# Optimization experiments

Measured on AMD Instinct MI355X. Metric: run time of the kernel, lower is better.

## Reference

```python
import jax, jax.numpy as jnp
import numpy as np

B, CIN, COUT, WID, M1, M2, H, W = 8, 3, 3, 16, 8, 8, 256, 256


def _fftfreq(n, d):
    # torch.fft.fftfreq(n, d); d may be a traced scalar
    k = np.concatenate([np.arange(0, (n - 1) // 2 + 1), np.arange(-(n // 2), 0)]).astype(np.float32)
    return jnp.asarray(k) / (n * d)


def _cplx(ri):
    return jax.lax.complex(ri[..., 0], ri[..., 1])


def _inorm(v, eps=1e-5):
    # InstanceNorm2d, affine=False: normalize over spatial dims per (b, c)
    mu = jnp.mean(v, axis=(-2, -1), keepdims=True)
    var = jnp.var(v, axis=(-2, -1), keepdims=True)
    return (v - mu) * jax.lax.rsqrt(var + eps)


def setup_inputs() -> dict:
    key = jax.random.key(0)
    ks = jax.random.split(key, 13)
    scale = 1.0 / (WID * WID)
    u = lambda k, s: scale * (0.5 + 0.5 * jax.random.uniform(k, s, jnp.float32))
    return {
        "x": jax.random.normal(ks[0], (B, CIN, H, W), jnp.float32),
        "fc0_w": jax.random.normal(ks[1], (CIN + 2, WID), jnp.float32) * 0.1,
        "fc0_b": jax.random.normal(ks[2], (WID,), jnp.float32) * 0.01,
        "pole1_ri": u(ks[3], (WID, WID, M1, 2)),
        "pole2_ri": u(ks[4], (WID, WID, M2, 2)),
        "residue_ri": u(ks[5], (WID, WID, M1, M2, 2)),
        "w0_w": jax.random.normal(ks[6], (WID, WID), jnp.float32) * 0.1,
        "w0_b": jax.random.normal(ks[7], (WID,), jnp.float32) * 0.01,
        "fc1_w": jax.random.normal(ks[8], (WID, 128), jnp.float32) * 0.1,
        "fc1_b": jax.random.normal(ks[9], (128,), jnp.float32) * 0.01,
        "fc2_w": jax.random.normal(ks[10], (128, COUT), jnp.float32) * 0.1,
        "fc2_b": jax.random.normal(ks[11], (COUT,), jnp.float32) * 0.01,
        "tx": jnp.linspace(0.0, 1.0, W, dtype=jnp.float32).reshape(1, W),
        "ty": jnp.linspace(0.0, 1.0, H, dtype=jnp.float32).reshape(1, H),
    }


def _pr2d(v, p1, p2, res, tx, ty):
    # v: [b, i, h, w] real; p1:[i,k,m1], p2:[i,k,m2], res:[i,k,m1,m2] complex
    b, i, h, w = v.shape
    dty = ty[0, 1] - ty[0, 0]
    dtx = tx[0, 1] - tx[0, 0]
    alpha = jnp.fft.fft2(v)  # [b,i,h,w] complex64
    lam1 = (2j * jnp.pi) * _fftfreq(h, dty)  # [h]
    lam2 = (2j * jnp.pi) * _fftfreq(w, dtx)  # [w]
    A1 = 1.0 / (lam1[None, None, None, :] - p1[..., None])  # [i,k,p,h]
    A2 = 1.0 / (lam2[None, None, None, :] - p2[..., None])  # [i,k,q,w]
    # output_residue1[b,k,o,x] = sum_{i,p,q} alpha[b,i,o,x] res[i,k,p,q] A1[i,k,p,o] A2[i,k,q,x]
    T = jnp.einsum('ikpq,ikpo->ikqo', res, A1)
    G = jnp.einsum('ikqo,ikqx->ikox', T, A2)        # [i,k,h,w] pole-residue transfer kernel
    out1 = jnp.einsum('biox,ikox->bkox', alpha, G)
    x1 = jnp.fft.ifft2(out1).real
    # output_residue2[b,k,p,q] = sum_{i,o,x} alpha[b,i,o,x] res[i,k,p,q] A1[i,k,p,o] A2[i,k,q,x]
    S = jnp.einsum('biox,ikqx->bikoq', alpha, A2)
    Mt = jnp.einsum('bikoq,ikpo->bikpq', S, A1)
    out2 = jnp.einsum('bikpq,ikpq->bkpq', Mt, res)  # [b,k,m1,m2]
    # transient part: x2[n,i,z,x] = sum_{b,p,q} out2[n,b,p,q] exp(p1[b,i,p] ty[z]) exp(p2[b,i,q] tx[x])
    tyc = ty.reshape(-1).astype(p1.dtype)
    txc = tx.reshape(-1).astype(p2.dtype)
    E1 = jnp.exp(p1[..., None] * tyc)  # [i,k,p,h]
    E2 = jnp.exp(p2[..., None] * txc)  # [i,k,q,w]
    U = jnp.einsum('nbpq,bipz->nbiqz', out2, E1)
    x2 = jnp.einsum('nbiqz,biqx->nizx', U, E2).real / (w * h)
    return x1 + x2


def reference(x, fc0_w, fc0_b, pole1_ri, pole2_ri, residue_ri, w0_w, w0_b,
              fc1_w, fc1_b, fc2_w, fc2_b, tx, ty):
    b, c, h, w = x.shape
    v = jnp.transpose(x, (0, 2, 3, 1))  # [b,h,w,c]
    gx = jnp.broadcast_to(jnp.linspace(0.0, 1.0, h, dtype=x.dtype)[None, :, None, None], (b, h, w, 1))
    gy = jnp.broadcast_to(jnp.linspace(0.0, 1.0, w, dtype=x.dtype)[None, None, :, None], (b, h, w, 1))
    v = jnp.concatenate([v, gx, gy], axis=-1)
    v = v @ fc0_w + fc0_b                 # [b,h,w,width]
    v = jnp.transpose(v, (0, 3, 1, 2))    # [b,width,h,w]
    p1, p2, res = _cplx(pole1_ri), _cplx(pole2_ri), _cplx(residue_ri)
    x1 = _inorm(_pr2d(_inorm(v), p1, p2, res, tx, ty))
    x2 = jnp.einsum('bihw,oi->bohw', v, w0_w) + w0_b[None, :, None, None]  # 1x1 conv
    u = x1 + x2
    u = jnp.transpose(u, (0, 2, 3, 1))
    u = jnp.sin(u @ fc1_w + fc1_b)
    u = u @ fc2_w + fc2_b
    return jnp.transpose(u, (0, 3, 1, 2))
```

## Files before the change

### kernel.cpp

```cpp
#include <hip/hip_runtime.h>
#include <cstddef>

#define NPIX 65536
#define PI_F 3.14159265358979323846f

__device__ __forceinline__ void cacc(float2& acc, float2 a, float2 b) {
  acc.x = fmaf(a.x, b.x, fmaf(-a.y, b.y, acc.x));
  acc.y = fmaf(a.x, b.y, fmaf(a.y, b.x, acc.y));
}
__device__ __forceinline__ float2 cmulf(float2 a, float2 b) {
  return make_float2(a.x*b.x - a.y*b.y, a.x*b.y + a.y*b.x);
}
__device__ __forceinline__ float2 add2(float2 a, float2 b) { return make_float2(a.x+b.x, a.y+b.y); }
__device__ __forceinline__ float2 sub2(float2 a, float2 b) { return make_float2(a.x-b.x, a.y-b.y); }
__device__ __forceinline__ float2 shflc(float2 v, int mask) {
  return make_float2(__shfl_xor(v.x, mask), __shfl_xor(v.y, mask));
}
__device__ __forceinline__ void make_tw(float sgn, int l, float2* tw) {
  const float c = sgn * (2.0f*PI_F/256.0f);
  int idxs[8] = { l, 64+l, 2*l, (l&31)<<2, (l&15)<<3, (l&7)<<4, (l&3)<<5, (l&1)<<6 };
  #pragma unroll
  for (int r = 0; r < 8; ++r) { float sn, cs; __sincosf(c*idxs[r], &sn, &cs); tw[r] = make_float2(cs, sn); }
}
__device__ __forceinline__ void fwd_stage(float2& vv, int lane, int H, float2 tws, bool unit) {
  float2 p = shflc(vv, H);
  bool up = (lane & H) != 0;
  float2 lo = add2(vv, p);
  float2 df = sub2(p, vv);
  float2 hi = unit ? df : cmulf(df, tws);
  vv = up ? hi : lo;
}
__device__ __forceinline__ void inv_stage(float2& vv, int lane, int H, float2 tws, bool unit) {
  float2 p = shflc(vv, H);
  bool up = (lane & H) != 0;
  float2 bv = up ? vv : p;
  float2 av = up ? p : vv;
  float2 t = unit ? bv : cmulf(bv, tws);
  vv = up ? sub2(av, t) : add2(av, t);
}
__device__ __forceinline__ void ifft256_reg(float2& v0, float2& v1, float2& v2,
    float2& v3, int lane, const float2* tw) {
  inv_stage(v0, lane, 1, tw[0], true ); inv_stage(v1, lane, 1, tw[0], true );
  inv_stage(v2, lane, 1, tw[0], true ); inv_stage(v3, lane, 1, tw[0], true );
  inv_stage(v0, lane, 2, tw[7], false); inv_stage(v1, lane, 2, tw[7], false);
  inv_stage(v2, lane, 2, tw[7], false); inv_stage(v3, lane, 2, tw[7], false);
  inv_stage(v0, lane, 4, tw[6], false); inv_stage(v1, lane, 4, tw[6], false);
  inv_stage(v2, lane, 4, tw[6], false); inv_stage(v3, lane, 4, tw[6], false);
  inv_stage(v0, lane, 8, tw[5], false); inv_stage(v1, lane, 8, tw[5], false);
  inv_stage(v2, lane, 8, tw[5], false); inv_stage(v3, lane, 8, tw[5], false);
  inv_stage(v0, lane, 16, tw[4], false); inv_stage(v1, lane, 16, tw[4], false);
  inv_stage(v2, lane, 16, tw[4], false); inv_stage(v3, lane, 16, tw[4], false);
  inv_stage(v0, lane, 32, tw[3], false); inv_stage(v1, lane, 32, tw[3], false);
  inv_stage(v2, lane, 32, tw[3], false); inv_stage(v3, lane, 32, tw[3], false);
  { float2 t01 = cmulf(v1, tw[2]); float2 n0 = add2(v0, t01), n1 = sub2(v0, t01);
    float2 t23 = cmulf(v3, tw[2]); float2 n2 = add2(v2, t23), n3 = sub2(v2, t23);
    v0 = n0; v1 = n1; v2 = n2; v3 = n3; }
  { float2 t02 = cmulf(v2, tw[0]); float2 n0 = add2(v0, t02), n2 = sub2(v0, t02);
    float2 t13 = cmulf(v3, tw[1]); float2 n1 = add2(v1, t13), n3 = sub2(v1, t13);
    v0 = n0; v2 = n2; v1 = n1; v3 = n3; }
}

__global__ __launch_bounds__(256) void k_setup(const float2* __restrict__ p1,
    const float2* __restrict__ p2, const float* __restrict__ txv,
    const float* __restrict__ tyv, float2* __restrict__ A1,
    float2* __restrict__ A2T, float2* __restrict__ A2L,
    float2* __restrict__ E1, float2* __restrict__ E2) {
  int gid = blockIdx.x*256 + threadIdx.x;
  int o = gid & 255, p = (gid>>8)&7, k = (gid>>11)&15, i = gid>>15;
  float ko = (o < 128) ? (float)o : (float)(o - 256);
  float dty = tyv[1] - tyv[0];
  float dtx = txv[1] - txv[0];
  const float TWO_PI = 6.283185307179586f;
  {
    float lam = TWO_PI * ko / (256.0f * dty);
    float2 pv = p1[(i*16+k)*8 + p];
    float xr = -pv.x, yi = lam - pv.y;
    float D = xr*xr + yi*yi;
    A1[((size_t)((i*16+k)*8 + p))*256 + o] = make_float2(xr/D, -yi/D);
    float tv = tyv[o];
    float m = expf(pv.x*tv);
    E1[((size_t)((i*16+k)*8 + p))*256 + o] = make_float2(m*cosf(pv.y*tv), m*sinf(pv.y*tv));
  }
  {
    int fo = __brev((unsigned)o) >> 24;
    float ko2 = (fo < 128) ? (float)fo : (float)(fo - 256);
    float lam = TWO_PI * ko2 / (256.0f * dtx);
    float2 pv = p2[(i*16+k)*8 + p];
    float xr = -pv.x, yi = lam - pv.y;
    float D = xr*xr + yi*yi;
    float2 val = make_float2(xr/D, -yi/D);
    A2T[((size_t)i*256 + o)*128 + k*8 + p] = val;
    A2L[((size_t)((i*16+k)*8 + p))*256 + o] = val;
    float tv = txv[o];
    float m = expf(pv.x*tv);
    E2[((size_t)((i*16+k)*8 + p))*256 + o] = make_float2(m*cosf(pv.y*tv), m*sinf(pv.y*tv));
  }
}

__global__ __launch_bounds__(256) void k_T(const float2* __restrict__ res,
    const float2* __restrict__ A1, float2* __restrict__ Tt) {
  int ik = blockIdx.x, tid = threadIdx.x;
  __shared__ float2 rbuf[64];
  __shared__ float2 a1[8][256];
  if (tid < 64) rbuf[tid] = res[(size_t)ik*64 + tid];
  for (int e = 0; e < 8; ++e) {
    int lin = tid + 256*e;
    int p = lin >> 8, o = lin & 255;
    a1[p][o] = A1[((size_t)ik*8 + p)*256 + o];
  }
  __syncthreads();
  int o = tid;
  #pragma unroll
  for (int q = 0; q < 8; ++q) {
    float2 acc = make_float2(0.f, 0.f);
    #pragma unroll
    for (int p = 0; p < 8; ++p) cacc(acc, rbuf[p*8+q], a1[p][o]);
    Tt[((size_t)ik*8 + q)*256 + o] = acc;
  }
}

__global__ __launch_bounds__(256) void k_stats_v_part(const float* __restrict__ x,
    const float* __restrict__ fc0w, const float* __restrict__ fc0b,
    float2* __restrict__ part) {
  int bid = blockIdx.x;
  int seg = bid & 7, img = bid >> 3;
  int k = img & 15, b = img >> 4;
  int tid = threadIdx.x;
  float w0 = fc0w[k], w1 = fc0w[16+k], w2 = fc0w[32+k], w3 = fc0w[48+k], w4 = fc0w[64+k];
  float base = fc0b[k] + (tid*(1.0f/255.0f))*w4;
  const float* xb = x + (size_t)b*3*NPIX + (size_t)seg*8192;
  float s = 0.f, s2 = 0.f;
  for (int it = 0; it < 32; ++it) {
    int row = seg*32 + it;
    int p = it*256 + tid;
    float val = base + (row*(1.0f/255.0f))*w3 + xb[p]*w0 + xb[NPIX+p]*w1 + xb[2*NPIX+p]*w2;
    s += val; s2 += val*val;
  }
  __shared__ float rs[256], rq[256];
  rs[tid] = s; rq[tid] = s2;
  __syncthreads();
  for (int off = 128; off > 0; off >>= 1) {
    if (tid < off) { rs[tid] += rs[tid+off]; rq[tid] += rq[tid+off]; }
    __syncthreads();
  }
  if (tid == 0) part[bid] = make_float2(rs[0], rq[0]);
}

__global__ __launch_bounds__(256) void k_stats_p_part(const float* __restrict__ v,
    float2* __restrict__ part) {
  int bid = blockIdx.x;
  int seg = bid & 7, img = bid >> 3;
  int tid = threadIdx.x;
  const float* p = v + (size_t)img*NPIX + (size_t)seg*8192;
  float s = 0.f, s2 = 0.f;
  for (int it = 0; it < 32; ++it) { float a = p[it*256 + tid]; s += a; s2 += a*a; }
  __shared__ float rs[256], rq[256];
  rs[tid] = s; rq[tid] = s2;
  __syncthreads();
  for (int off = 128; off > 0; off >>= 1) {
    if (tid < off) { rs[tid] += rs[tid+off]; rq[tid] += rq[tid+off]; }
    __syncthreads();
  }
  if (tid == 0) part[bid] = make_float2(rs[0], rq[0]);
}

__global__ __launch_bounds__(256) void k_stats_fin(const float2* __restrict__ part,
    float2* __restrict__ stats, int nimg) {
  int img = blockIdx.x*256 + threadIdx.x;
  if (img >= nimg) return;
  float s = 0.f, s2 = 0.f;
  #pragma unroll
  for (int e = 0; e < 8; ++e) { float2 v = part[img*8 + e]; s += v.x; s2 += v.y; }
  float mean = s * (1.0f/65536.0f);
  float var  = s2 * (1.0f/65536.0f) - mean*mean;
  stats[img] = make_float2(mean, rsqrtf(var + 1e-5f));
}

__global__ __launch_bounds__(256) void k_fft_v(const float* __restrict__ x,
    const float* __restrict__ fc0w, const float* __restrict__ fc0b,
    const float2* __restrict__ stats, float2* __restrict__ out) {
  int tid = threadIdx.x, lane = tid & 63, rowi = tid >> 6;
  int bid = blockIdx.x;
  int img = bid >> 6;
  int h   = (bid & 63)*4 + rowi;
  int k = img & 15, b = img >> 4;
  float2 st = stats[img];
  float w0 = fc0w[k], w1 = fc0w[16+k], w2 = fc0w[32+k], w3 = fc0w[48+k], w4 = fc0w[64+k];
  float bb = fc0b[k] + (h*(1.0f/255.0f))*w3;
  const float* xb = x + (size_t)b*3*NPIX + (size_t)h*256;
  float2 tw[8];
  make_tw(-1.0f, lane, tw);
  float2 v0, v1, v2, v3;
  {
    #pragma unroll
    for (int e = 0; e < 4; ++e) {
      int j = e*64 + lane;
      float val = bb + (j*(1.0f/255.0f))*w4 + xb[j]*w0 + xb[NPIX+j]*w1 + xb[2*NPIX+j]*w2;
      val = (val - st.x)*st.y;
      float2 c = make_float2(val, 0.f);
      if (e == 0) v0 = c; else if (e == 1) v1 = c; else if (e == 2) v2 = c; else v3 = c;
    }
  }
  { float2 n0 = add2(v0, v2), n2 = cmulf(sub2(v0, v2), tw[0]);
    float2 n1 = add2(v1, v3), n3 = cmulf(sub2(v1, v3), tw[1]);
    v0 = n0; v1 = n1; v2 = n2; v3 = n3; }
  { float2 n0 = add2(v0, v1), n1 = cmulf(sub2(v0, v1), tw[2]);
    float2 n2 = add2(v2, v3), n3 = cmulf(sub2(v2, v3), tw[2]);
    v0 = n0; v1 = n1; v2 = n2; v3 = n3; }
  fwd_stage(v0, lane, 32, tw[3], false); fwd_stage(v1, lane, 32, tw[3], false);
  fwd_stage(v2, lane, 32, tw[3], false); fwd_stage(v3, lane, 32, tw[3], false);
  fwd_stage(v0, lane, 16, tw[4], false); fwd_stage(v1, lane, 16, tw[4], false);
  fwd_stage(v2, lane, 16, tw[4], false); fwd_stage(v3, lane, 16, tw[4], false);
  fwd_stage(v0, lane,  8, tw[5], false); fwd_stage(v1, lane,  8, tw[5], false);
  fwd_stage(v2, lane,  8, tw[5], false); fwd_stage(v3, lane,  8, tw[5], false);
  fwd_stage(v0, lane,  4, tw[6], false); fwd_stage(v1, lane,  4, tw[6], false);
  fwd_stage(v2, lane,  4, tw[6], false); fwd_stage(v3, lane,  4, tw[6], false);
  fwd_stage(v0, lane,  2, tw[7], false); fwd_stage(v1, lane,  2, tw[7], false);
  fwd_stage(v2, lane,  2, tw[7], false); fwd_stage(v3, lane,  2, tw[7], false);
  fwd_stage(v0, lane,  1, tw[0], true ); fwd_stage(v1, lane,  1, tw[0], true );
  fwd_stage(v2, lane,  1, tw[0], true ); fwd_stage(v3, lane,  1, tw[0], true );
  float2* op = out + ((size_t)img*256 + h)*256;
  op[lane] = v0; op[64+lane] = v1; op[128+lane] = v2; op[192+lane] = v3;
}

__global__ __launch_bounds__(256) void k_fft_colR(const float2* __restrict__ in,
    float2* __restrict__ outp) {
  __shared__ float tr[256][17], tim[256][17];
  __shared__ float twr[128], twi[128];
  int tid = threadIdx.x;
  int c = tid & 15, g = tid >> 4;
  int img = blockIdx.x >> 4;
  int c0  = (blockIdx.x & 15) * 16;
  if (tid < 128) {
    float ang = (PI_F/128.0f)*tid;
    twr[tid] = cosf(ang); twi[tid] = -sinf(ang);
  }
  const float2* base = in + (size_t)img*NPIX + c0;
  #pragma unroll
  for (int it = 0; it < 16; ++it) {
    int row = it*16 + g;
    float2 v = base[(size_t)row*256 + c];
    int br = __brev((unsigned)row) >> 24;
    tr[br][c] = v.x; tim[br][c] = v.y;
  }
  __syncthreads();
  int lane = tid & 63, w = tid >> 6;
  int cw = w*4 + (lane >> 4);
  int gw = lane & 15;
  for (int s = 0; s < 8; ++s) {
    __builtin_amdgcn_wave_barrier();
    int half = 1 << s;
    #pragma unroll
    for (int r = 0; r < 8; ++r) {
      int m  = gw + 16*r;
      int t  = m & (half - 1);
      int grp = m >> s;
      int i0 = (grp << (s+1)) + t;
      int i1 = i0 + half;
      int twx = t << (7 - s);
      float wr = twr[twx], wi = twi[twx];
      float br = tr[i1][cw], bi = tim[i1][cw];
      float vr = br*wr - bi*wi, vi = br*wi + bi*wr;
      float ar = tr[i0][cw], ai = tim[i0][cw];
      tr[i0][cw] = ar + vr; tim[i0][cw] = ai + vi;
      tr[i1][cw] = ar - vr; tim[i1][cw] = ai - vi;
    }
  }
  __syncthreads();
  #pragma unroll
  for (int it = 0; it < 16; ++it) {
    int row = it*16 + g;
    outp[((size_t)row*128 + img)*256 + c0 + c] = make_float2(tr[row][c], tim[row][c]);
  }
}

__global__ __launch_bounds__(256) void k_ifft_col_real(const float2* __restrict__ in,
    float* __restrict__ outp, float scale) {
  __shared__ float tr[256][17], tim[256][17];
  __shared__ float twr[128], twi[128];
  int tid = threadIdx.x;
  int c = tid & 15, g = tid >> 4;
  int img = blockIdx.x >> 4;
  int c0  = (blockIdx.x & 15) * 16;
  if (tid < 128) {
    float ang = (PI_F/128.0f)*tid;
    twr[tid] = cosf(ang); twi[tid] = sinf(ang);
  }
  const float2* base = in + (size_t)img*NPIX + c0;
  #pragma unroll
  for (int it = 0; it < 16; ++it) {
    int row = it*16 + g;
    float2 v = base[(size_t)row*256 + c];
    int br = __brev((unsigned)row) >> 24;
    tr[br][c] = v.x; tim[br][c] = v.y;
  }
  __syncthreads();
  int lane = tid & 63, w = tid >> 6;
  int cw = w*4 + (lane >> 4);
  int gw = lane & 15;
  for (int s = 0; s < 8; ++s) {
    __builtin_amdgcn_wave_barrier();
    int half = 1 << s;
    #pragma unroll
    for (int r = 0; r < 8; ++r) {
      int m  = gw + 16*r;
      int t  = m & (half - 1);
      int grp = m >> s;
      int i0 = (grp << (s+1)) + t;
      int i1 = i0 + half;
      int twx = t << (7 - s);
      float wr = twr[twx], wi = twi[twx];
      float br = tr[i1][cw], bi = tim[i1][cw];
      float vr = br*wr - bi*wi, vi = br*wi + bi*wr;
      float ar = tr[i0][cw], ai = tim[i0][cw];
      tr[i0][cw] = ar + vr; tim[i0][cw] = ai + vi;
      tr[i1][cw] = ar - vr; tim[i1][cw] = ai - vi;
    }
  }
  __syncthreads();
  float* ob = outp + (size_t)img*NPIX + c0;
  #pragma unroll
  for (int it = 0; it < 16; ++it) {
    int row = it*16 + g;
    ob[(size_t)row*256 + c] = tr[row][c]*scale;
  }
}

__global__ __launch_bounds__(256) void k_S(const float2* __restrict__ alphaR,
    const float2* __restrict__ A2T, float2* __restrict__ S) {
  __shared__ float2 al[16][256];
  int bid = blockIdx.x;
  int oblk = bid & 15, ni = bid >> 4;
  int i = ni & 15;
  int tid = threadIdx.x;
  for (int r = 0; r < 16; ++r)
    al[r][tid] = alphaR[((size_t)(oblk*16 + r)*128 + ni)*256 + tid];
  __syncthreads();
  int j = tid & 127, oh = tid >> 7;
  float2 acc[8];
  #pragma unroll
  for (int ol = 0; ol < 8; ++ol) acc[ol] = make_float2(0.f, 0.f);
  const float2* a2p = A2T + (size_t)i*32768 + j;
  float2 p0 = a2p[0], p1 = a2p[128], p2 = a2p[256], p3 = a2p[384];
  for (int xx = 0; xx < 256; xx += 4) {
    float2 a0 = p0, a1 = p1, a2v = p2, a3 = p3;
    int nx = xx + 4;
    if (nx < 256) {
      p0 = a2p[(size_t)nx*128];       p1 = a2p[(size_t)(nx+1)*128];
      p2 = a2p[(size_t)(nx+2)*128];   p3 = a2p[(size_t)(nx+3)*128];
    }
    #pragma unroll
    for (int ol = 0; ol < 8; ++ol) {
      const float4* rp = reinterpret_cast<const float4*>(&al[oh*8+ol][xx]);
      float4 v01 = rp[0], v23 = rp[1];
      cacc(acc[ol], make_float2(v01.x, v01.y), a0);
      cacc(acc[ol], make_float2(v01.z, v01.w), a1);
      cacc(acc[ol], make_float2(v23.x, v23.y), a2v);
      cacc(acc[ol], make_float2(v23.z, v23.w), a3);
    }
  }
  #pragma unroll
  for (int ol = 0; ol < 8; ++ol) {
    int o = oblk*16 + oh*8 + ol;
    S[((size_t)ni*256 + o)*128 + j] = acc[ol];
  }
}

__global__ __launch_bounds__(256) void k_Mt(const float2* __restrict__ S,
    const float2* __restrict__ A1, float2* __restrict__ Mt) {
  __shared__ float2 sl[8][258];
  __shared__ float2 a1l[8][258];
  __shared__ float2 part[4][64];
  int bid = blockIdx.x;
  int k = bid & 15, ni = bid >> 4;
  int i = ni & 15;
  int ik = i*16 + k;
  int tid = threadIdx.x;
  for (int e = 0; e < 8; ++e) {
    int lin = tid + 256*e;
    int o = lin >> 3, q = lin & 7;
    sl[q][o] = S[((size_t)ni*256 + o)*128 + k*8 + q];
  }
  for (int e = 0; e < 8; ++e) {
    int lin = tid + 256*e;
    int p = lin >> 8, o = lin & 255;
    a1l[p][o] = A1[((size_t)ik*8 + p)*256 + o];
  }
  __syncthreads();
  int oq = tid >> 6, pq = tid & 63, p = pq >> 3, q = pq & 7;
  float2 acc = make_float2(0.f, 0.f);
  int o0 = oq*64;
  for (int o = o0; o < o0 + 64; ++o) cacc(acc, sl[q][o], a1l[p][o]);
  part[oq][pq] = acc;
  __syncthreads();
  if (oq == 0) {
    float2 a = part[0][pq], b = part[1][pq], c = part[2][pq], d = part[3][pq];
    acc.x = a.x + b.x + c.x + d.x;
    acc.y = a.y + b.y + c.y + d.y;
    Mt[(size_t)bid*64 + pq] = acc;
  }
}

__global__ __launch_bounds__(256) void k_out2(const float2* __restrict__ Mt,
    const float2* __restrict__ res, float2* __restrict__ out2) {
  int gid = blockIdx.x*256 + threadIdx.x;
  int pq = gid & 63, k = (gid >> 6) & 15, n = gid >> 10;
  float2 acc = make_float2(0.f, 0.f);
  for (int i = 0; i < 16; ++i)
    cacc(acc, Mt[((size_t)((n*16+i)*16 + k))*64 + pq], res[((size_t)(i*16+k))*64 + pq]);
  out2[((size_t)(n*16+k))*64 + pq] = acc;
}

__global__ __launch_bounds__(256) void k_out1g(const float2* __restrict__ alphaR,
    const float2* __restrict__ Tt, const float2* __restrict__ A2L,
    float2* __restrict__ out1) {
  __shared__ float2 tl[2][128];
  __shared__ float sre[4][256], sim[4][256];
  int d = blockIdx.x;
  int xcd = d & 7, idx = d >> 3;
  int o  = xcd*32 + (idx >> 3);
  int kh = idx & 7;
  int tid = threadIdx.x, x = tid;
  int lane = tid & 63, rowi = tid >> 6;
  {
    int kk = tid >> 7, rem = tid & 127;
    int i = rem >> 3, q = rem & 7;
    tl[kk][rem] = Tt[((size_t)((i*16 + 2*kh + kk)*8 + q))*256 + o];
  }
  float2 tw[8];
  make_tw(+1.0f, lane, tw);
  __syncthreads();
  float2 g0[16], g1[16];
  #pragma unroll
  for (int i = 0; i < 16; ++i) {
    const float2* a2k0 = &A2L[((size_t)((i*16 + 2*kh + 0)*8))*256 + x];
    const float2* a2k1 = &A2L[((size_t)((i*16 + 2*kh + 1)*8))*256 + x];
    float2 acc0 = make_float2(0.f, 0.f), acc1 = make_float2(0.f, 0.f);
    #pragma unroll
    for (int q = 0; q < 8; ++q) {
      cacc(acc0, tl[0][i*8+q], a2k0[(size_t)q*256]);
      cacc(acc1, tl[1][i*8+q], a2k1[(size_t)q*256]);
    }
    g0[i] = acc0; g1[i] = acc1;
  }
  const float2* arow = alphaR + (size_t)o*128*256 + x;
  float2 arA[16], arB[16];
  #pragma unroll
  for (int i = 0; i < 16; ++i) arA[i] = arow[(size_t)(0*16 + i)*256];
  #pragma unroll
  for (int i = 0; i < 16; ++i) arB[i] = arow[(size_t)(1*16 + i)*256];
  for (int bp = 0; bp < 4; ++bp) {
    float2 acc0 = make_float2(0.f,0.f), acc1 = acc0, acc2 = acc0, acc3 = acc0;
    #pragma unroll
    for (int i = 0; i < 16; ++i) {
      cacc(acc0, arA[i], g0[i]);
      cacc(acc1, arA[i], g1[i]);
      cacc(acc2, arB[i], g0[i]);
      cacc(acc3, arB[i], g1[i]);
    }
    sre[0][x] = acc0.x; sim[0][x] = acc0.y;
    sre[1][x] = acc1.x; sim[1][x] = acc1.y;
    sre[2][x] = acc2.x; sim[2][x] = acc2.y;
    sre[3][x] = acc3.x; sim[3][x] = acc3.y;
    __syncthreads();
    if (bp < 3) {
      int b0 = (bp+1)*2, b1 = b0 + 1;
      #pragma unroll
      for (int i = 0; i < 16; ++i) arA[i] = arow[(size_t)(b0*16 + i)*256];
      #pragma unroll
      for (int i = 0; i < 16; ++i) arB[i] = arow[(size_t)(b1*16 + i)*256];
    }
    float2 v0 = make_float2(sre[rowi][lane],     sim[rowi][lane]);
    float2 v1 = make_float2(sre[rowi][64+lane],  sim[rowi][64+lane]);
    float2 v2 = make_float2(sre[rowi][128+lane], sim[rowi][128+lane]);
    float2 v3 = make_float2(sre[rowi][192+lane], sim[rowi][192+lane]);
    ifft256_reg(v0, v1, v2, v3, lane, tw);
    int img = (bp*2 + (rowi >> 1))*16 + 2*kh + (rowi & 1);
    float2* op = out1 + ((size_t)img*256 + o)*256;
    op[lane] = v0; op[64+lane] = v1; op[128+lane] = v2; op[192+lane] = v3;
    __syncthreads();
  }
}

__global__ __launch_bounds__(256) void k_x2t(const float2* __restrict__ out2,
    const float2* __restrict__ E1, const float2* __restrict__ E2,
    float* __restrict__ x1pre) {
  int bid = blockIdx.x;
  int zb = bid & 31, nk = bid >> 5;
  int kk = nk & 15, n = nk >> 4;
  int x = threadIdx.x;
  __shared__ float2 o2[1024];
  __shared__ float2 e1l[1024];
  __shared__ float2 ul[1024];
  for (int e = 0; e < 4; ++e) {
    int lin = threadIdx.x + 256*e;
    int j = lin >> 6, pq = lin & 63;
    o2[lin] = out2[((size_t)(n*16 + j))*64 + pq];
  }
  for (int e = 0; e < 4; ++e) {
    int lin = threadIdx.x + 256*e;
    int j = lin >> 6, p = (lin >> 3) & 7, zz = lin & 7;
    e1l[lin] = E1[(((size_t)(j*16 + kk))*8 + p)*256 + zb*8 + zz];
  }
  __syncthreads();
  for (int e = 0; e < 4; ++e) {
    int lin = threadIdx.x + 256*e;
    int j = lin >> 6, q = (lin >> 3) & 7, zz = lin & 7;
    float2 acc = make_float2(0.f, 0.f);
    #pragma unroll
    for (int p = 0; p < 8; ++p) cacc(acc, o2[j*64 + p*8 + q], e1l[j*64 + p*8 + zz]);
    ul[lin] = acc;
  }
  __syncthreads();
  float acc[8] = {0.f,0.f,0.f,0.f,0.f,0.f,0.f,0.f};
  const float2* e2b = E2 + (size_t)kk*2048 + x;
  float2 nxt = e2b[0];
  for (int jq = 0; jq < 128; ++jq) {
    float2 e2 = nxt;
    int njq = jq + 1;
    if (njq < 128) {
      int nj = njq >> 3, nq = njq & 7;
      nxt = e2b[(size_t)nj*32768 + (size_t)nq*256];
    }
    const float4* up4 = reinterpret_cast<const float4*>(&ul[jq*8]);
    float4 u01 = up4[0], u23 = up4[1], u45 = up4[2], u67 = up4[3];
    acc[0] = fmaf(u01.x, e2.x, fmaf(-u01.y, e2.y, acc[0]));
    acc[1] = fmaf(u01.z, e2.x, fmaf(-u01.w, e2.y, acc[1]));
    acc[2] = fmaf(u23.x, e2.x, fmaf(-u23.y, e2.y, acc[2]));
    acc[3] = fmaf(u23.z, e2.x, fmaf(-u23.w, e2.y, acc[3]));
    acc[4] = fmaf(u45.x, e2.x, fmaf(-u45.y, e2.y, acc[4]));
    acc[5] = fmaf(u45.z, e2.x, fmaf(-u45.w, e2.y, acc[5]));
    acc[6] = fmaf(u67.x, e2.x, fmaf(-u67.y, e2.y, acc[6]));
    acc[7] = fmaf(u67.z, e2.x, fmaf(-u67.w, e2.y, acc[7]));
  }
  const float sc = 1.0f/65536.0f;
  #pragma unroll
  for (int zz = 0; zz < 8; ++zz) {
    size_t idx = (((size_t)nk)*256 + zb*8 + zz)*256 + x;
    x1pre[idx] += acc[zz]*sc;
  }
}

__global__ __launch_bounds__(256) void k_final(const float* __restrict__ x,
    const float* __restrict__ x1pre, const float2* __restrict__ stats2,
    const float* __restrict__ fc0w, const float* __restrict__ fc0b,
    const float* __restrict__ w0w, const float* __restrict__ w0b,
    const float* __restrict__ fc1w, const float* __restrict__ fc1b,
    const float* __restrict__ fc2w, const float* __restrict__ fc2b,
    float* __restrict__ out) {
  __shared__ float s_fc1w[2048], s_fc1b[128], s_fc2w[384], s_w0w[256], s_w0b[16], s_fc2b[3];
  int tid = threadIdx.x;
  for (int e = 0; e < 8; ++e) s_fc1w[tid + 256*e] = fc1w[tid + 256*e];
  if (tid < 128) s_fc1b[tid] = fc1b[tid];
  for (int e = 0; e < 2; ++e) { int q = tid + 256*e; if (q < 384) s_fc2w[q] = fc2w[q]; }
  s_w0w[tid] = w0w[tid];
  if (tid < 16) s_w0b[tid] = w0b[tid];
  if (tid < 3)  s_fc2b[tid] = fc2b[tid];
  __syncthreads();

  int bid = blockIdx.x;
  int hh = bid & 255, b = bid >> 8;
  int ww = tid;
  size_t pix = (size_t)hh*256 + ww;
  float xc0 = x[((size_t)b*3 + 0)*NPIX + pix];
  float xc1 = x[((size_t)b*3 + 1)*NPIX + pix];
  float xc2 = x[((size_t)b*3 + 2)*NPIX + pix];
  float gx = hh*(1.0f/255.0f), gy = ww*(1.0f/255.0f);
  float v[16], x1n[16], uo[16];
  #pragma unroll
  for (int k = 0; k < 16; ++k)
    v[k] = fc0b[k] + xc0*fc0w[k] + xc1*fc0w[16+k] + xc2*fc0w[32+k] + gx*fc0w[48+k] + gy*fc0w[64+k];
  #pragma unroll
  for (int k = 0; k < 16; ++k) {
    float2 st = stats2[b*16 + k];
    float xv = x1pre[((size_t)(b*16 + k))*NPIX + pix];
    x1n[k] = (xv - st.x)*st.y;
  }
  #pragma unroll
  for (int o = 0; o < 16; ++o) {
    float acc = s_w0b[o];
    #pragma unroll
    for (int k = 0; k < 16; ++k) acc = fmaf(v[k], s_w0w[o*16+k], acc);
    uo[o] = acc + x1n[o];
  }
  float o0 = 0.f, o1 = 0.f, o2 = 0.f;
  for (int jj = 0; jj < 128; ++jj) {
    float t = s_fc1b[jj];
    #pragma unroll
    for (int k = 0; k < 16; ++k) t = fmaf(uo[k], s_fc1w[k*128 + jj], t);
    float s = __sinf(t);
    o0 = fmaf(s, s_fc2w[jj*3+0], o0);
    o1 = fmaf(s, s_fc2w[jj*3+1], o1);
    o2 = fmaf(s, s_fc2w[jj*3+2], o2);
  }
  out[((size_t)b*3 + 0)*NPIX + pix] = o0 + s_fc2b[0];
  out[((size_t)b*3 + 1)*NPIX + pix] = o1 + s_fc2b[1];
  out[((size_t)b*3 + 2)*NPIX + pix] = o2 + s_fc2b[2];
}

extern "C" void kernel_launch(void* const* d_in, const int* in_sizes, int n_in,
                              void* d_out, int out_size, void* d_ws, size_t ws_size,
                              hipStream_t stream) {
  const float*  x    = (const float*)d_in[0];
  const float*  fc0w = (const float*)d_in[1];
  const float*  fc0b = (const float*)d_in[2];
  const float2* p1   = (const float2*)d_in[3];
  const float2* p2   = (const float2*)d_in[4];
  const float2* res  = (const float2*)d_in[5];
  const float*  w0w  = (const float*)d_in[6];
  const float*  w0b  = (const float*)d_in[7];
  const float*  fc1w = (const float*)d_in[8];
  const float*  fc1b = (const float*)d_in[9];
  const float*  fc2w = (const float*)d_in[10];
  const float*  fc2b = (const float*)d_in[11];
  const float*  txv  = (const float*)d_in[12];
  const float*  tyv  = (const float*)d_in[13];
  float* out = (float*)d_out;

  const size_t OFF_A1   = 0;
  const size_t OFF_A2T  = 4194304;
  const size_t OFF_E1   = 8388608;
  const size_t OFF_E2   = 12582912;
  const size_t OFF_ST1  = 16777216;
  const size_t OFF_ST2  = 16778240;
  const size_t OFF_OUT2 = 16779264;
  const size_t OFF_MT   = 16844800;
  const size_t OFF_S    = 17893376;
  const size_t OFF_X1   = 51447808;
  const size_t OFF_A    = 85002240;
  const size_t OFF_B    = 152111104;
  const size_t OFF_G    = 219219968;
  const size_t NEED     = 252774400;
  if (ws_size < NEED) return;
  char* ws = (char*)d_ws;
  float2* A1  = (float2*)(ws + OFF_A1);
  float2* A2T = (float2*)(ws + OFF_A2T);
  float2* E1  = (float2*)(ws + OFF_E1);
  float2* E2  = (float2*)(ws + OFF_E2);
  float2* st1 = (float2*)(ws + OFF_ST1);
  float2* st2 = (float2*)(ws + OFF_ST2);
  float2* o2b = (float2*)(ws + OFF_OUT2);
  float2* Mt  = (float2*)(ws + OFF_MT);
  float2* Sb  = (float2*)(ws + OFF_S);
  float2* Tt  = (float2*)(ws + OFF_X1);
  float*  X1  = (float*)(ws + OFF_X1);
  float2* Ab  = (float2*)(ws + OFF_A);
  float2* Bb  = (float2*)(ws + OFF_B);
  float2* A2L = (float2*)(ws + OFF_G);

  k_setup  <<<2048, 256, 0, stream>>>(p1, p2, txv, tyv, A1, A2T, A2L, E1, E2);
  k_T      <<<256, 256, 0, stream>>>(res, A1, Tt);
  k_stats_v_part<<<1024, 256, 0, stream>>>(x, fc0w, fc0b, Sb);
  k_stats_fin   <<<1, 256, 0, stream>>>(Sb, st1, 128);
  k_fft_v  <<<8192, 256, 0, stream>>>(x, fc0w, fc0b, st1, Ab);
  k_fft_colR<<<2048, 256, 0, stream>>>(Ab, Bb);
  k_S      <<<2048, 256, 0, stream>>>(Bb, A2T, Sb);
  k_Mt     <<<2048, 256, 0, stream>>>(Sb, A1, Mt);
  k_out2   <<<32, 256, 0, stream>>>(Mt, res, o2b);
  k_out1g  <<<2048, 256, 0, stream>>>(Bb, Tt, A2L, Ab);
  k_ifft_col_real<<<2048, 256, 0, stream>>>(Ab, X1, 1.0f/65536.0f);
  k_x2t    <<<4096, 256, 0, stream>>>(o2b, E1, E2, X1);
  k_stats_p_part<<<1024, 256, 0, stream>>>(X1, Sb);
  k_stats_fin   <<<1, 256, 0, stream>>>(Sb, st2, 128);
  k_final  <<<2048, 256, 0, stream>>>(x, X1, st2, fc0w, fc0b,
                                      w0w, w0b, fc1w, fc1b, fc2w, fc2b, out);
}
```

Baseline: 564.6 us.

## Replace scalar complex contraction in k_S with split-bf16 MFMA GEMM

Rewrites the alpha-by-A2 complex contraction as a real GEMM on matrix cores. The complex operands are expanded into real/imag interleaved form, and each float is split into high and low bf16 parts. Three bf16 MFMAs per tile (hi*hi, lo*hi, hi*lo) approximate fp32 accuracy. A new k_B kernel prepacks the A2T operand into bf16 hi/lo buffers, and the output layout is written so downstream k_Mt reads the same complex layout. The aim is to cut the FP32 FMA cost of k_S, at the price of extra packing work and some precision loss from the three-term bf16 split.

```diff
diff --git a/kernel.cpp b/kernel.cpp
--- a/kernel.cpp
+++ b/kernel.cpp
@@ -3,6 +3,10 @@
 
 #define NPIX 65536
 #define PI_F 3.14159265358979323846f
+
+typedef float v4f __attribute__((ext_vector_type(4)));
+typedef short v8s __attribute__((ext_vector_type(8)));
+typedef unsigned short u16;
 
 __device__ __forceinline__ void cacc(float2& acc, float2 a, float2 b) {
   acc.x = fmaf(a.x, b.x, fmaf(-a.y, b.y, acc.x));
@@ -15,6 +19,12 @@
 __device__ __forceinline__ float2 sub2(float2 a, float2 b) { return make_float2(a.x-b.x, a.y-b.y); }
 __device__ __forceinline__ float2 shflc(float2 v, int mask) {
   return make_float2(__shfl_xor(v.x, mask), __shfl_xor(v.y, mask));
+}
+__device__ __forceinline__ void bf16split(float v, u16& h, u16& l) {
+  unsigned bits = __float_as_uint(v);
+  h = (u16)(bits >> 16);
+  float r = v - __uint_as_float((unsigned)h << 16);
+  l = (u16)(__float_as_uint(r) >> 16);
 }
 __device__ __forceinline__ void make_tw(float sgn, int l, float2* tw) {
   const float c = sgn * (2.0f*PI_F/256.0f);
@@ -97,6 +107,28 @@
   }
 }
 
+__global__ __launch_bounds__(256) void k_B(const float2* __restrict__ A2T,
+    u16* __restrict__ BH, u16* __restrict__ BL) {
+  int bid = blockIdx.x;
+  int i = bid >> 3, g = bid & 7;
+  int tid = threadIdx.x;
+  int n2 = g*32 + (tid >> 3);
+  int kq = n2 >> 1, par = n2 & 1;
+  int x0 = (tid & 7) * 32;
+  size_t outb = ((size_t)i*256 + n2)*512;
+  for (int xx = 0; xx < 32; ++xx) {
+    int x = x0 + xx;
+    float2 a2 = A2T[((size_t)i*256 + x)*128 + kq];
+    float v0 = par ? a2.y : a2.x;
+    float v1 = par ? a2.x : -a2.y;
+    u16 h0, l0, h1, l1;
+    bf16split(v0, h0, l0);
+    bf16split(v1, h1, l1);
+    BH[outb + 2*x]     = h0;  BL[outb + 2*x]     = l0;
+    BH[outb + 2*x + 1] = h1;  BL[outb + 2*x + 1] = l1;
+  }
+}
+
 __global__ __launch_bounds__(256) void k_T(const float2* __restrict__ res,
     const float2* __restrict__ A1, float2* __restrict__ Tt) {
   int ik = blockIdx.x, tid = threadIdx.x;
@@ -326,43 +358,80 @@
   }
 }
 
-__global__ __launch_bounds__(256) void k_S(const float2* __restrict__ alphaR,
-    const float2* __restrict__ A2T, float2* __restrict__ S) {
-  __shared__ float2 al[16][256];
+__global__ __launch_bounds__(256) void k_Smm(const float2* __restrict__ alphaR,
+    const u16* __restrict__ BH, const u16* __restrict__ BL,
+    float* __restrict__ Sf) {
+  __shared__ u16 Ah[128][40], Al[128][40], Bhs[128][40], Bls[128][40];
   int bid = blockIdx.x;
-  int oblk = bid & 15, ni = bid >> 4;
-  int i = ni & 15;
+  int i = bid >> 5, rem = bid & 31, mt = rem >> 1, nt = rem & 1;
   int tid = threadIdx.x;
-  for (int r = 0; r < 16; ++r)
-    al[r][tid] = alphaR[((size_t)(oblk*16 + r)*128 + ni)*256 + tid];
-  __syncthreads();
-  int j = tid & 127, oh = tid >> 7;
-  float2 acc[8];
-  #pragma unroll
-  for (int ol = 0; ol < 8; ++ol) acc[ol] = make_float2(0.f, 0.f);
-  const float2* a2p = A2T + (size_t)i*32768 + j;
-  float2 p0 = a2p[0], p1 = a2p[128], p2 = a2p[256], p3 = a2p[384];
-  for (int xx = 0; xx < 256; xx += 4) {
-    float2 a0 = p0, a1 = p1, a2v = p2, a3 = p3;
-    int nx = xx + 4;
-    if (nx < 256) {
-      p0 = a2p[(size_t)nx*128];       p1 = a2p[(size_t)(nx+1)*128];
-      p2 = a2p[(size_t)(nx+2)*128];   p3 = a2p[(size_t)(nx+3)*128];
-    }
-    #pragma unroll
-    for (int ol = 0; ol < 8; ++ol) {
-      const float4* rp = reinterpret_cast<const float4*>(&al[oh*8+ol][xx]);
-      float4 v01 = rp[0], v23 = rp[1];
-      cacc(acc[ol], make_float2(v01.x, v01.y), a0);
-      cacc(acc[ol], make_float2(v01.z, v01.w), a1);
-      cacc(acc[ol], make_float2(v23.x, v23.y), a2v);
-      cacc(acc[ol], make_float2(v23.z, v23.w), a3);
-    }
-  }
-  #pragma unroll
-  for (int ol = 0; ol < 8; ++ol) {
-    int o = oblk*16 + oh*8 + ol;
-    S[((size_t)ni*256 + o)*128 + j] = acc[ol];
+  int lane = tid & 63, wid = tid >> 6, wr = wid >> 1, wc = wid & 1;
+  int r2 = tid >> 1, h2 = tid & 1;
+  int m_s = mt*128 + r2;
+  const float2* arow = alphaR + ((size_t)((m_s & 255)*128) + (size_t)((m_s >> 8)*16 + i))*256 + h2*8;
+  const u16* bhrow = BH + ((size_t)i*256 + nt*128 + r2)*512 + h2*16;
+  const u16* blrow = BL + ((size_t)i*256 + nt*128 + r2)*512 + h2*16;
+  v4f acc[4][4];
+  #pragma unroll
+  for (int a = 0; a < 4; ++a)
+    #pragma unroll
+    for (int b = 0; b < 4; ++b) acc[a][b] = (v4f){0.f, 0.f, 0.f, 0.f};
+  for (int kc = 0; kc < 16; ++kc) {
+    const float2* ap = arow + kc*16;
+    #pragma unroll
+    for (int e = 0; e < 8; ++e) {
+      float2 v = ap[e];
+      u16 hr, lr, hi_, li_;
+      bf16split(v.x, hr, lr);
+      bf16split(v.y, hi_, li_);
+      int c = h2*16 + 2*e;
+      Ah[r2][c] = hr; Ah[r2][c+1] = hi_;
+      Al[r2][c] = lr; Al[r2][c+1] = li_;
+    }
+    {
+      const uint4* ph = (const uint4*)(bhrow + (size_t)kc*32);
+      uint4 q0 = ph[0], q1 = ph[1];
+      *((uint4*)&Bhs[r2][h2*16])     = q0;
+      *((uint4*)&Bhs[r2][h2*16 + 8]) = q1;
+      const uint4* pl = (const uint4*)(blrow + (size_t)kc*32);
+      uint4 s0 = pl[0], s1 = pl[1];
+      *((uint4*)&Bls[r2][h2*16])     = s0;
+      *((uint4*)&Bls[r2][h2*16 + 8]) = s1;
+    }
+    __syncthreads();
+    v8s af_h[4], af_l[4];
+    int c8 = (lane >> 4) * 8;
+    #pragma unroll
+    for (int fi = 0; fi < 4; ++fi) {
+      int row = wr*64 + fi*16 + (lane & 15);
+      af_h[fi] = *(const v8s*)&Ah[row][c8];
+      af_l[fi] = *(const v8s*)&Al[row][c8];
+    }
+    #pragma unroll
+    for (int fj = 0; fj < 4; ++fj) {
+      int row = wc*64 + fj*16 + (lane & 15);
+      v8s bh_f = *(const v8s*)&Bhs[row][c8];
+      v8s bl_f = *(const v8s*)&Bls[row][c8];
+      #pragma unroll
+      for (int fi = 0; fi < 4; ++fi) {
+        acc[fi][fj] = __builtin_amdgcn_mfma_f32_16x16x32_bf16(af_h[fi], bh_f, acc[fi][fj], 0, 0, 0);
+        acc[fi][fj] = __builtin_amdgcn_mfma_f32_16x16x32_bf16(af_l[fi], bh_f, acc[fi][fj], 0, 0, 0);
+        acc[fi][fj] = __builtin_amdgcn_mfma_f32_16x16x32_bf16(af_h[fi], bl_f, acc[fi][fj], 0, 0, 0);
+      }
+    }
+    __syncthreads();
+  }
+  #pragma unroll
+  for (int fi = 0; fi < 4; ++fi) {
+    #pragma unroll
+    for (int rr = 0; rr < 4; ++rr) {
+      int m = mt*128 + wr*64 + fi*16 + (lane >> 4)*4 + rr;
+      int n = m >> 8, o = m & 255;
+      float* srow = Sf + ((size_t)(n*16 + i)*256 + o)*256 + nt*128 + wc*64 + (lane & 15);
+      #pragma unroll
+      for (int fj = 0; fj < 4; ++fj)
+        srow[fj*16] = acc[fi][fj][rr];
+    }
   }
 }
 
@@ -647,14 +716,17 @@
   float2* Ab  = (float2*)(ws + OFF_A);
   float2* Bb  = (float2*)(ws + OFF_B);
   float2* A2L = (float2*)(ws + OFF_G);
+  u16*    BH  = (u16*)(ws + OFF_G + 4194304);
+  u16*    BL  = (u16*)(ws + OFF_G + 8388608);
 
   k_setup  <<<2048, 256, 0, stream>>>(p1, p2, txv, tyv, A1, A2T, A2L, E1, E2);
+  k_B      <<<128, 256, 0, stream>>>(A2T, BH, BL);
   k_T      <<<256, 256, 0, stream>>>(res, A1, Tt);
   k_stats_v_part<<<1024, 256, 0, stream>>>(x, fc0w, fc0b, Sb);
   k_stats_fin   <<<1, 256, 0, stream>>>(Sb, st1, 128);
   k_fft_v  <<<8192, 256, 0, stream>>>(x, fc0w, fc0b, st1, Ab);
   k_fft_colR<<<2048, 256, 0, stream>>>(Ab, Bb);
-  k_S      <<<2048, 256, 0, stream>>>(Bb, A2T, Sb);
+  k_Smm    <<<512, 256, 0, stream>>>(Bb, BH, BL, (float*)Sb);
   k_Mt     <<<2048, 256, 0, stream>>>(Sb, A1, Mt);
   k_out2   <<<32, 256, 0, stream>>>(Mt, res, o2b);
   k_out1g  <<<2048, 256, 0, stream>>>(Bb, Tt, A2L, Ab);
```

Result: faster. 512.7 us (-9.2%).
